# Performance work log

Measured on AMD Instinct MI355X. Metric: run time of the kernel, lower is better.

Reference implementation:

```python
import jax, jax.numpy as jnp
import numpy as np

N_NODES = 80000
N_EDGES = 1280000
IN_C, HID_C, OUT_C = 128, 64, 40


def setup_inputs() -> dict:
    key = jax.random.key(0)
    k1, k2, k3, k4 = jax.random.split(key, 4)
    x = jax.random.normal(k1, (N_NODES, IN_C), dtype=jnp.float32)
    edge_index = jax.random.randint(k2, (2, N_EDGES), 0, N_NODES, dtype=jnp.int32)
    W1 = jax.random.normal(k3, (IN_C, HID_C), dtype=jnp.float32) * (1.0 / np.sqrt(IN_C))
    W2 = jax.random.normal(k4, (HID_C, OUT_C), dtype=jnp.float32) * (1.0 / np.sqrt(HID_C))
    return {"x": x, "edge_index": edge_index, "W1": W1, "W2": W2}


def _spmm_add(edge_index, h):
    # adj_t.matmul(h): out[dst] += h[src]  (aggr='add', message = x_j)
    src, dst = edge_index[0], edge_index[1]
    return jax.ops.segment_sum(h[src], dst, num_segments=N_NODES)


def reference(x, edge_index, W1, W2):
    # GCNConv 1: linear (no bias) then add-aggregate SpMM
    h = _spmm_add(edge_index, x @ W1)          # [N, HID]
    h = jax.nn.relu(h)
    # GCNConv 2
    h = _spmm_add(edge_index, h @ W2)          # [N, OUT]
    return jax.nn.log_softmax(h, axis=-1)
```

## Files before the change

kernel.cpp:

```cpp
#include <hip/hip_runtime.h>
#include <hip/hip_bf16.h>
#include <math.h>

#define N_NODES 80000
#define N_EDGES 1280000
#define IN_C 128
#define HID_C 64
#define OUT_C 40

#define KB 313
#define BK_CAP 4600
#define EPT_A 8

__device__ __forceinline__ float bf_lo(unsigned u) {
    union { unsigned i; float f; } c; c.i = u << 16; return c.f;
}
__device__ __forceinline__ float bf_hi(unsigned u) {
    union { unsigned i; float f; } c; c.i = u & 0xffff0000u; return c.f;
}
__device__ __forceinline__ unsigned pack_bf2(float a, float b) {
    union { float f; unsigned i; } ca, cb; ca.f = a; cb.f = b;
    unsigned ra = (ca.i + 0x7fffu + ((ca.i >> 16) & 1u)) >> 16;
    unsigned rb = (cb.i + 0x7fffu + ((cb.i >> 16) & 1u)) >> 16;
    return ra | (rb << 16);
}

typedef short v8s __attribute__((ext_vector_type(8)));
typedef float v4f __attribute__((ext_vector_type(4)));
typedef float v2f __attribute__((ext_vector_type(2)));
union U16 { uint4 u; v8s s; };

__device__ __forceinline__ v2f bf2f(unsigned u) {
    return (v2f){bf_lo(u), bf_hi(u)};
}
__device__ __forceinline__ void acc_fp8x4(float* a, unsigned u) {
    const v2f lo = __builtin_amdgcn_cvt_pk_f32_fp8((int)u, false);
    const v2f hi = __builtin_amdgcn_cvt_pk_f32_fp8((int)u, true);
    a[0] += lo[0]; a[1] += lo[1]; a[2] += hi[0]; a[3] += hi[1];
}

__global__ void prep_w_kernel(const float* __restrict__ W1, const float* __restrict__ W2,
                              unsigned* __restrict__ w1t, unsigned* __restrict__ w2t,
                              int* __restrict__ bcnt) {
    const int tid = threadIdx.x;
    for (int i = tid; i < KB; i += 256) bcnt[i] = 0;
    for (int i = tid; i < 4096; i += 256) {
        const int wcol = i >> 6, kk = i & 63;
        w1t[i] = pack_bf2(W1[(2 * kk) * HID_C + wcol], W1[(2 * kk + 1) * HID_C + wcol]);
    }
    for (int i = tid; i < 1536; i += 256) {
        const int wcol = i >> 5, kk = i & 31;
        w2t[i] = (wcol < OUT_C)
            ? pack_bf2(W2[(2 * kk) * OUT_C + wcol], W2[(2 * kk + 1) * OUT_C + wcol])
            : 0u;
    }
}

__global__ __launch_bounds__(512) void binA_kernel(const int* __restrict__ src,
                                                   const int* __restrict__ dst,
                                                   int* __restrict__ bcnt,
                                                   int* __restrict__ gbuf) {
    __shared__ int lcnt[KB];
    __shared__ int lexcl[KB];
    __shared__ int lbase[KB];
    __shared__ int lcur[KB];
    __shared__ int stage[512 * EPT_A];
    __shared__ int gaddr[512 * EPT_A];
    const int tid = threadIdx.x;

    for (int i = tid; i < KB; i += 512) lcnt[i] = 0;
    __syncthreads();

    const int e0 = blockIdx.x * 512 * EPT_A;
    int my_s[EPT_A], my_b[EPT_A], my_dl[EPT_A];
#pragma unroll
    for (int j = 0; j < EPT_A; ++j) {
        const int e = e0 + j * 512 + tid;
        if (e < N_EDGES) {
            const int d = dst[e];
            my_s[j] = src[e];
            my_b[j] = d >> 8;
            my_dl[j] = d & 255;
            atomicAdd(&lcnt[my_b[j]], 1);
        } else my_b[j] = -1;
    }
    __syncthreads();

    if (tid < KB) lexcl[tid] = lcnt[tid];
    __syncthreads();
    for (int o = 1; o < KB; o <<= 1) {
        int t = (tid < KB && tid >= o) ? lexcl[tid - o] : 0;
        __syncthreads();
        if (tid < KB) lexcl[tid] += t;
        __syncthreads();
    }
    const int total = lexcl[KB - 1];
    if (tid < KB) {
        lexcl[tid] -= lcnt[tid];
        lbase[tid] = (lcnt[tid] > 0) ? atomicAdd(&bcnt[tid], lcnt[tid]) : 0;
        lcur[tid] = 0;
    }
    __syncthreads();

#pragma unroll
    for (int j = 0; j < EPT_A; ++j) {
        if (my_b[j] >= 0) {
            const int b = my_b[j];
            const int r = atomicAdd(&lcur[b], 1);
            const int li = lexcl[b] + r;
            stage[li] = (my_s[j] << 8) | my_dl[j];
            int gp = lbase[b] + r;
            if (gp >= BK_CAP) gp = BK_CAP - 1;
            gaddr[li] = b * BK_CAP + gp;
        }
    }
    __syncthreads();

    for (int i = tid; i < total; i += 512)
        gbuf[gaddr[i]] = stage[i];
}

__global__ __launch_bounds__(512) void binB_kernel(const int* __restrict__ bcnt,
                                                   const int* __restrict__ gbuf,
                                                   int* __restrict__ rp,
                                                   int* __restrict__ col) {
    __shared__ int sc[KB];
    __shared__ int hist[256];
    __shared__ int excl[256];
    __shared__ int cur[256];
    __shared__ int outb[BK_CAP];
    const int b = blockIdx.x;
    const int tid = threadIdx.x;

    if (tid < KB) sc[tid] = min(bcnt[tid], BK_CAP);
    __syncthreads();
    for (int o = 1; o < KB; o <<= 1) {
        int t = (tid < KB && tid >= o) ? sc[tid - o] : 0;
        __syncthreads();
        if (tid < KB) sc[tid] += t;
        __syncthreads();
    }
    const int n = min(bcnt[b], BK_CAP);
    const int cbase = sc[b] - n;
    const int* __restrict__ my = gbuf + (size_t)b * BK_CAP;

    if (tid < 256) hist[tid] = 0;
    __syncthreads();
    for (int i = tid; i < n; i += 512)
        atomicAdd(&hist[my[i] & 255], 1);
    __syncthreads();

    int h = 0, psv = 0;
    if (tid < 256) { h = hist[tid]; psv = h; excl[tid] = h; }
    __syncthreads();
    for (int o = 1; o < 256; o <<= 1) {
        int t = (tid < 256 && tid >= o) ? excl[tid - o] : 0;
        __syncthreads();
        if (tid < 256) excl[tid] += t;
        __syncthreads();
    }
    if (tid < 256) {
        const int ex = excl[tid] - h;
        cur[tid] = ex;
        const int node = b * 256 + tid;
        if (node <= N_NODES) rp[node] = cbase + ex;
        excl[tid] = ex;
    }
    __syncthreads();

    for (int i = tid; i < n; i += 512) {
        const int pk = my[i];
        const int pos = atomicAdd(&cur[pk & 255], 1);
        outb[pos] = pk >> 8;
    }
    __syncthreads();
    for (int i = tid; i < n; i += 512)
        col[cbase + i] = outb[i];
}

__global__ __launch_bounds__(256) void gemm1_kernel(const float* __restrict__ x,
                                                    const unsigned* __restrict__ w1t,
                                                    unsigned* __restrict__ h1b) {
    const int wave = threadIdx.x >> 6, lane = threadIdx.x & 63;
    const int nl = lane & 15, quad = lane >> 4;
    const int node = (blockIdx.x * 4 + wave) * 16 + nl;

    v4f acc[4];
#pragma unroll
    for (int q = 0; q < 4; ++q) acc[q] = (v4f){0.f, 0.f, 0.f, 0.f};

#pragma unroll
    for (int kit = 0; kit < 4; ++kit) {
        const float* xp = x + (size_t)node * IN_C + kit * 32 + quad * 8;
        const float4 lo = *(const float4*)xp;
        const float4 hi = *(const float4*)(xp + 4);
        U16 bu;
        bu.u.x = pack_bf2(lo.x, lo.y); bu.u.y = pack_bf2(lo.z, lo.w);
        bu.u.z = pack_bf2(hi.x, hi.y); bu.u.w = pack_bf2(hi.z, hi.w);
#pragma unroll
        for (int mt = 0; mt < 4; ++mt) {
            U16 au;
            au.u = *(const uint4*)(w1t + ((mt * 16 + nl) * 64 + kit * 16 + quad * 4));
            acc[mt] = __builtin_amdgcn_mfma_f32_16x16x32_bf16(au.s, bu.s, acc[mt], 0, 0, 0);
        }
    }
#pragma unroll
    for (int mt = 0; mt < 4; ++mt) {
        uint2 o;
        o.x = pack_bf2(acc[mt][0], acc[mt][1]);
        o.y = pack_bf2(acc[mt][2], acc[mt][3]);
        *(uint2*)(h1b + (size_t)node * 32 + mt * 8 + quad * 2) = o;
    }
}

__global__ void gather64_kernel(const int* __restrict__ rp, const int* __restrict__ col,
                                const unsigned* __restrict__ h1b,
                                unsigned* __restrict__ agg1b) {
    const int lane = threadIdx.x & 63;
    const int wave = threadIdx.x >> 6;
    const int sl = lane & 31;
    const int es = sl >> 3;
    const int cl = sl & 7;
    const int gbase = lane & 32;
    const int node = blockIdx.x * 8 + wave * 2 + (lane >> 5);
    const int b = rp[node], e = rp[node + 1];

    v2f acc[4];
#pragma unroll
    for (int k = 0; k < 4; ++k) acc[k] = (v2f){0.f, 0.f};

    for (int pos = b; __any(pos < e); pos += 32) {
        const int rem = e - pos;
        const int n = rem > 32 ? 32 : (rem > 0 ? rem : 0);
        const int myIdx = (sl < n) ? col[pos + sl] : 0;
        const int steps = (n + 3) >> 2;
        int j = 0;
        for (; j + 1 < steps; j += 2) {
            const int e0 = (j << 2) + es, e1 = e0 + 4;
            const int s0 = __shfl(myIdx, gbase + e0, 64);
            const int s1 = __shfl(myIdx, gbase + e1, 64);
            uint4 v0, v1;
            const bool g0 = e0 < n, g1 = e1 < n;
            if (g0) v0 = *(const uint4*)(h1b + (size_t)s0 * 32 + cl * 4);
            if (g1) v1 = *(const uint4*)(h1b + (size_t)s1 * 32 + cl * 4);
            if (g0) {
                acc[0] += bf2f(v0.x); acc[1] += bf2f(v0.y);
                acc[2] += bf2f(v0.z); acc[3] += bf2f(v0.w);
            }
            if (g1) {
                acc[0] += bf2f(v1.x); acc[1] += bf2f(v1.y);
                acc[2] += bf2f(v1.z); acc[3] += bf2f(v1.w);
            }
        }
        if (j < steps) {
            const int e0 = (j << 2) + es;
            const int s0 = __shfl(myIdx, gbase + e0, 64);
            if (e0 < n) {
                const uint4 v = *(const uint4*)(h1b + (size_t)s0 * 32 + cl * 4);
                acc[0] += bf2f(v.x); acc[1] += bf2f(v.y);
                acc[2] += bf2f(v.z); acc[3] += bf2f(v.w);
            }
        }
    }
#pragma unroll
    for (int k = 0; k < 4; ++k) {
        acc[k][0] += __shfl_down(acc[k][0], 16, 64);
        acc[k][1] += __shfl_down(acc[k][1], 16, 64);
    }
#pragma unroll
    for (int k = 0; k < 4; ++k) {
        acc[k][0] += __shfl_down(acc[k][0], 8, 64);
        acc[k][1] += __shfl_down(acc[k][1], 8, 64);
    }

    if (sl < 8) {
        uint4 o;
        o.x = pack_bf2(fmaxf(acc[0][0], 0.f), fmaxf(acc[0][1], 0.f));
        o.y = pack_bf2(fmaxf(acc[1][0], 0.f), fmaxf(acc[1][1], 0.f));
        o.z = pack_bf2(fmaxf(acc[2][0], 0.f), fmaxf(acc[2][1], 0.f));
        o.w = pack_bf2(fmaxf(acc[3][0], 0.f), fmaxf(acc[3][1], 0.f));
        *(uint4*)(agg1b + (size_t)node * 32 + cl * 4) = o;
    }
}

__global__ __launch_bounds__(256) void gemm2_kernel(const unsigned* __restrict__ agg1b,
                                                    const unsigned* __restrict__ w2t,
                                                    unsigned* __restrict__ h2f) {
    const int wave = threadIdx.x >> 6, lane = threadIdx.x & 63;
    const int nl = lane & 15, quad = lane >> 4;
    const int node = (blockIdx.x * 4 + wave) * 16 + nl;

    v4f c[3];
#pragma unroll
    for (int q = 0; q < 3; ++q) c[q] = (v4f){0.f, 0.f, 0.f, 0.f};

#pragma unroll
    for (int kit = 0; kit < 2; ++kit) {
        U16 bu;
        bu.u = *(const uint4*)(agg1b + (size_t)node * 32 + kit * 16 + quad * 4);
#pragma unroll
        for (int mt = 0; mt < 3; ++mt) {
            U16 au;
            au.u = *(const uint4*)(w2t + ((mt * 16 + nl) * 32 + kit * 16 + quad * 4));
            c[mt] = __builtin_amdgcn_mfma_f32_16x16x32_bf16(au.s, bu.s, c[mt], 0, 0, 0);
        }
    }
#pragma unroll
    for (int mt = 0; mt < 3; ++mt) {
        const int idx = mt * 4 + quad;
        if (idx < 10) {
            int u = 0;
            u = __builtin_amdgcn_cvt_pk_fp8_f32(c[mt][0], c[mt][1], u, false);
            u = __builtin_amdgcn_cvt_pk_fp8_f32(c[mt][2], c[mt][3], u, true);
            h2f[(size_t)node * 10 + idx] = (unsigned)u;
        }
    }
}

__global__ void gather40_ls_kernel(const int* __restrict__ rp, const int* __restrict__ col,
                                   const unsigned* __restrict__ h2f,
                                   float* __restrict__ out) {
    const int lane = threadIdx.x & 63;
    const int wave = threadIdx.x >> 6;
    const int sl = lane & 15;
    const int es = sl / 5;
    const int cl = sl - es * 5;
    const int gbase = lane & 48;
    const int node = blockIdx.x * 16 + wave * 4 + (lane >> 4);
    const int b = rp[node], e = rp[node + 1];

    float a[8];
#pragma unroll
    for (int k = 0; k < 8; ++k) a[k] = 0.f;

    for (int pos = b; __any(pos < e); pos += 16) {
        const int rem = e - pos;
        const int n = rem > 16 ? 16 : (rem > 0 ? rem : 0);
        const int myIdx = (sl < n) ? col[pos + sl] : 0;
#pragma unroll
        for (int j = 0; j < 6; ++j) {
            const int ei = j * 3 + es;
            const int s = __shfl(myIdx, gbase + ei, 64);
            if ((es < 3) && (ei < n)) {
                const uint2 v = *(const uint2*)(h2f + (size_t)s * 10 + cl * 2);
                acc_fp8x4(a, v.x);
                acc_fp8x4(a + 4, v.y);
            }
        }
    }
#pragma unroll
    for (int k = 0; k < 8; ++k) {
        const float u = __shfl_down(a[k], 5, 64);
        const float w = __shfl_down(a[k], 10, 64);
        a[k] += u + w;
    }

    const bool own = sl < 5;
    float m = -INFINITY;
    if (own) {
        m = a[0];
#pragma unroll
        for (int k = 1; k < 8; ++k) m = fmaxf(m, a[k]);
    }
    const float m0 = __shfl(m, gbase + 0, 64), m1 = __shfl(m, gbase + 1, 64);
    const float m2 = __shfl(m, gbase + 2, 64), m3 = __shfl(m, gbase + 3, 64);
    const float m4 = __shfl(m, gbase + 4, 64);
    const float gm = fmaxf(fmaxf(fmaxf(m0, m1), fmaxf(m2, m3)), m4);

    float s = 0.f;
    if (own) {
#pragma unroll
        for (int k = 0; k < 8; ++k) s += __expf(a[k] - gm);
    }
    const float s0 = __shfl(s, gbase + 0, 64), s1 = __shfl(s, gbase + 1, 64);
    const float s2 = __shfl(s, gbase + 2, 64), s3 = __shfl(s, gbase + 3, 64);
    const float s4 = __shfl(s, gbase + 4, 64);
    const float ls = __logf(s0 + s1 + s2 + s3 + s4) + gm;

    if (own) {
        float* op = out + (size_t)node * OUT_C + cl * 8;
        *(float4*)op = make_float4(a[0] - ls, a[1] - ls, a[2] - ls, a[3] - ls);
        *(float4*)(op + 4) = make_float4(a[4] - ls, a[5] - ls, a[6] - ls, a[7] - ls);
    }
}

extern "C" void kernel_launch(void* const* d_in, const int* in_sizes, int n_in,
                              void* d_out, int out_size, void* d_ws, size_t ws_size,
                              hipStream_t stream) {
    const float* x  = (const float*)d_in[0];
    const int* eidx = (const int*)d_in[1];
    const float* W1 = (const float*)d_in[2];
    const float* W2 = (const float*)d_in[3];
    float* out = (float*)d_out;

    const int* src = eidx;
    const int* dst = eidx + N_EDGES;

    unsigned* h1b   = (unsigned*)d_ws;
    unsigned* agg1b = h1b + (size_t)N_NODES * 32;
    unsigned* h2f   = agg1b + (size_t)N_NODES * 32;
    int*      gbuf  = (int*)(h2f + (size_t)N_NODES * 10);
    int*      col   = gbuf + (size_t)KB * BK_CAP;
    int*      rp    = col + N_EDGES;
    int*      bcnt  = rp + (N_NODES + 1);
    unsigned* w1t   = (unsigned*)(bcnt + KB);
    unsigned* w2t   = w1t + 4096;

    prep_w_kernel<<<1, 256, 0, stream>>>(W1, W2, w1t, w2t, bcnt);
    binA_kernel<<<(N_EDGES + 512 * EPT_A - 1) / (512 * EPT_A), 512, 0, stream>>>(src, dst, bcnt, gbuf);
    binB_kernel<<<KB, 512, 0, stream>>>(bcnt, gbuf, rp, col);

    gemm1_kernel<<<N_NODES / 64, 256, 0, stream>>>(x, w1t, h1b);
    gather64_kernel<<<N_NODES / 8, 256, 0, stream>>>(rp, col, h1b, agg1b);
    gemm2_kernel<<<N_NODES / 64, 256, 0, stream>>>(agg1b, w2t, h2f);
    gather40_ls_kernel<<<N_NODES / 16, 256, 0, stream>>>(rp, col, h2f, out);
}
```

Baseline: 181.9 us.

## Fuse gemm1 into binning kernel, parallelize weight prep, simplify gather index loads

Merges the first GEMM into the edge-binning launch as extra blocks, so the two independent phases run concurrently and one launch is dropped. Weight preprocessing is spread over 16 blocks instead of one. Both gather kernels now read column indices straight from global memory per edge with a fixed unroll, replacing the cooperative load-and-shuffle. The fused kernel reserves large shared memory for gemm blocks that never use it, which may limit occupancy, and per-lane index loads add redundant memory traffic.

```diff
diff --git a/kernel.cpp b/kernel.cpp
--- a/kernel.cpp
+++ b/kernel.cpp
@@ -11,6 +11,8 @@
 #define KB 313
 #define BK_CAP 4600
 #define EPT_A 8
+#define BINA_BLOCKS 313
+#define GEMM1_BLOCKS 625
 
 __device__ __forceinline__ float bf_lo(unsigned u) {
     union { unsigned i; float f; } c; c.i = u << 16; return c.f;
@@ -33,33 +35,29 @@
 __device__ __forceinline__ v2f bf2f(unsigned u) {
     return (v2f){bf_lo(u), bf_hi(u)};
 }
-__device__ __forceinline__ void acc_fp8x4(float* a, unsigned u) {
-    const v2f lo = __builtin_amdgcn_cvt_pk_f32_fp8((int)u, false);
-    const v2f hi = __builtin_amdgcn_cvt_pk_f32_fp8((int)u, true);
-    a[0] += lo[0]; a[1] += lo[1]; a[2] += hi[0]; a[3] += hi[1];
-}
 
 __global__ void prep_w_kernel(const float* __restrict__ W1, const float* __restrict__ W2,
                               unsigned* __restrict__ w1t, unsigned* __restrict__ w2t,
                               int* __restrict__ bcnt) {
-    const int tid = threadIdx.x;
-    for (int i = tid; i < KB; i += 256) bcnt[i] = 0;
-    for (int i = tid; i < 4096; i += 256) {
-        const int wcol = i >> 6, kk = i & 63;
-        w1t[i] = pack_bf2(W1[(2 * kk) * HID_C + wcol], W1[(2 * kk + 1) * HID_C + wcol]);
-    }
-    for (int i = tid; i < 1536; i += 256) {
-        const int wcol = i >> 5, kk = i & 31;
-        w2t[i] = (wcol < OUT_C)
+    const int g = blockIdx.x * 256 + threadIdx.x;
+    if (g < KB) bcnt[g] = 0;
+    {
+        const int wcol = g >> 6, kk = g & 63;
+        w1t[g] = pack_bf2(W1[(2 * kk) * HID_C + wcol], W1[(2 * kk + 1) * HID_C + wcol]);
+    }
+    if (g < 1536) {
+        const int wcol = g >> 5, kk = g & 31;
+        w2t[g] = (wcol < OUT_C)
             ? pack_bf2(W2[(2 * kk) * OUT_C + wcol], W2[(2 * kk + 1) * OUT_C + wcol])
             : 0u;
     }
 }
 
-__global__ __launch_bounds__(512) void binA_kernel(const int* __restrict__ src,
-                                                   const int* __restrict__ dst,
-                                                   int* __restrict__ bcnt,
-                                                   int* __restrict__ gbuf) {
+__global__ __launch_bounds__(512) void binA_gemm1_kernel(
+        const int* __restrict__ src, const int* __restrict__ dst,
+        int* __restrict__ bcnt, int* __restrict__ gbuf,
+        const float* __restrict__ x, const unsigned* __restrict__ w1t,
+        unsigned* __restrict__ h1b) {
     __shared__ int lcnt[KB];
     __shared__ int lexcl[KB];
     __shared__ int lbase[KB];
@@ -67,6 +65,41 @@
     __shared__ int stage[512 * EPT_A];
     __shared__ int gaddr[512 * EPT_A];
     const int tid = threadIdx.x;
+
+    if (blockIdx.x >= BINA_BLOCKS) {
+        const int bid = blockIdx.x - BINA_BLOCKS;
+        const int wave = tid >> 6, lane = tid & 63;
+        const int nl = lane & 15, quad = lane >> 4;
+        const int node = (bid * 8 + wave) * 16 + nl;
+
+        v4f acc[4];
+#pragma unroll
+        for (int q = 0; q < 4; ++q) acc[q] = (v4f){0.f, 0.f, 0.f, 0.f};
+
+#pragma unroll
+        for (int kit = 0; kit < 4; ++kit) {
+            const float* xp = x + (size_t)node * IN_C + kit * 32 + quad * 8;
+            const float4 lo = *(const float4*)xp;
+            const float4 hi = *(const float4*)(xp + 4);
+            U16 bu;
+            bu.u.x = pack_bf2(lo.x, lo.y); bu.u.y = pack_bf2(lo.z, lo.w);
+            bu.u.z = pack_bf2(hi.x, hi.y); bu.u.w = pack_bf2(hi.z, hi.w);
+#pragma unroll
+            for (int mt = 0; mt < 4; ++mt) {
+                U16 au;
+                au.u = *(const uint4*)(w1t + ((mt * 16 + nl) * 64 + kit * 16 + quad * 4));
+                acc[mt] = __builtin_amdgcn_mfma_f32_16x16x32_bf16(au.s, bu.s, acc[mt], 0, 0, 0);
+            }
+        }
+#pragma unroll
+        for (int mt = 0; mt < 4; ++mt) {
+            uint2 o;
+            o.x = pack_bf2(acc[mt][0], acc[mt][1]);
+            o.y = pack_bf2(acc[mt][2], acc[mt][3]);
+            *(uint2*)(h1b + (size_t)node * 32 + mt * 8 + quad * 2) = o;
+        }
+        return;
+    }
 
     for (int i = tid; i < KB; i += 512) lcnt[i] = 0;
     __syncthreads();
@@ -150,8 +183,8 @@
         atomicAdd(&hist[my[i] & 255], 1);
     __syncthreads();
 
-    int h = 0, psv = 0;
-    if (tid < 256) { h = hist[tid]; psv = h; excl[tid] = h; }
+    int h = 0;
+    if (tid < 256) { h = hist[tid]; excl[tid] = h; }
     __syncthreads();
     for (int o = 1; o < 256; o <<= 1) {
         int t = (tid < 256 && tid >= o) ? excl[tid - o] : 0;
@@ -164,7 +197,6 @@
         cur[tid] = ex;
         const int node = b * 256 + tid;
         if (node <= N_NODES) rp[node] = cbase + ex;
-        excl[tid] = ex;
     }
     __syncthreads();
 
@@ -176,41 +208,6 @@
     __syncthreads();
     for (int i = tid; i < n; i += 512)
         col[cbase + i] = outb[i];
-}
-
-__global__ __launch_bounds__(256) void gemm1_kernel(const float* __restrict__ x,
-                                                    const unsigned* __restrict__ w1t,
-                                                    unsigned* __restrict__ h1b) {
-    const int wave = threadIdx.x >> 6, lane = threadIdx.x & 63;
-    const int nl = lane & 15, quad = lane >> 4;
-    const int node = (blockIdx.x * 4 + wave) * 16 + nl;
-
-    v4f acc[4];
-#pragma unroll
-    for (int q = 0; q < 4; ++q) acc[q] = (v4f){0.f, 0.f, 0.f, 0.f};
-
-#pragma unroll
-    for (int kit = 0; kit < 4; ++kit) {
-        const float* xp = x + (size_t)node * IN_C + kit * 32 + quad * 8;
-        const float4 lo = *(const float4*)xp;
-        const float4 hi = *(const float4*)(xp + 4);
-        U16 bu;
-        bu.u.x = pack_bf2(lo.x, lo.y); bu.u.y = pack_bf2(lo.z, lo.w);
-        bu.u.z = pack_bf2(hi.x, hi.y); bu.u.w = pack_bf2(hi.z, hi.w);
-#pragma unroll
-        for (int mt = 0; mt < 4; ++mt) {
-            U16 au;
-            au.u = *(const uint4*)(w1t + ((mt * 16 + nl) * 64 + kit * 16 + quad * 4));
-            acc[mt] = __builtin_amdgcn_mfma_f32_16x16x32_bf16(au.s, bu.s, acc[mt], 0, 0, 0);
-        }
-    }
-#pragma unroll
-    for (int mt = 0; mt < 4; ++mt) {
-        uint2 o;
-        o.x = pack_bf2(acc[mt][0], acc[mt][1]);
-        o.y = pack_bf2(acc[mt][2], acc[mt][3]);
-        *(uint2*)(h1b + (size_t)node * 32 + mt * 8 + quad * 2) = o;
-    }
 }
 
 __global__ void gather64_kernel(const int* __restrict__ rp, const int* __restrict__ col,
@@ -221,7 +218,6 @@
     const int sl = lane & 31;
     const int es = sl >> 3;
     const int cl = sl & 7;
-    const int gbase = lane & 32;
     const int node = blockIdx.x * 8 + wave * 2 + (lane >> 5);
     const int b = rp[node], e = rp[node + 1];
 
@@ -230,33 +226,12 @@
     for (int k = 0; k < 4; ++k) acc[k] = (v2f){0.f, 0.f};
 
     for (int pos = b; __any(pos < e); pos += 32) {
-        const int rem = e - pos;
-        const int n = rem > 32 ? 32 : (rem > 0 ? rem : 0);
-        const int myIdx = (sl < n) ? col[pos + sl] : 0;
-        const int steps = (n + 3) >> 2;
-        int j = 0;
-        for (; j + 1 < steps; j += 2) {
-            const int e0 = (j << 2) + es, e1 = e0 + 4;
-            const int s0 = __shfl(myIdx, gbase + e0, 64);
-            const int s1 = __shfl(myIdx, gbase + e1, 64);
-            uint4 v0, v1;
-            const bool g0 = e0 < n, g1 = e1 < n;
-            if (g0) v0 = *(const uint4*)(h1b + (size_t)s0 * 32 + cl * 4);
-            if (g1) v1 = *(const uint4*)(h1b + (size_t)s1 * 32 + cl * 4);
-            if (g0) {
-                acc[0] += bf2f(v0.x); acc[1] += bf2f(v0.y);
-                acc[2] += bf2f(v0.z); acc[3] += bf2f(v0.w);
-            }
-            if (g1) {
-                acc[0] += bf2f(v1.x); acc[1] += bf2f(v1.y);
-                acc[2] += bf2f(v1.z); acc[3] += bf2f(v1.w);
-            }
-        }
-        if (j < steps) {
-            const int e0 = (j << 2) + es;
-            const int s0 = __shfl(myIdx, gbase + e0, 64);
-            if (e0 < n) {
-                const uint4 v = *(const uint4*)(h1b + (size_t)s0 * 32 + cl * 4);
+#pragma unroll
+        for (int j = 0; j < 8; ++j) {
+            const int ei = pos + (j << 2) + es;
+            if (ei < e) {
+                const int s = col[ei];
+                const uint4 v = *(const uint4*)(h1b + (size_t)s * 32 + cl * 4);
                 acc[0] += bf2f(v.x); acc[1] += bf2f(v.y);
                 acc[2] += bf2f(v.z); acc[3] += bf2f(v.w);
             }
@@ -329,38 +304,39 @@
     const int node = blockIdx.x * 16 + wave * 4 + (lane >> 4);
     const int b = rp[node], e = rp[node + 1];
 
-    float a[8];
-#pragma unroll
-    for (int k = 0; k < 8; ++k) a[k] = 0.f;
-
-    for (int pos = b; __any(pos < e); pos += 16) {
-        const int rem = e - pos;
-        const int n = rem > 16 ? 16 : (rem > 0 ? rem : 0);
-        const int myIdx = (sl < n) ? col[pos + sl] : 0;
-#pragma unroll
-        for (int j = 0; j < 6; ++j) {
-            const int ei = j * 3 + es;
-            const int s = __shfl(myIdx, gbase + ei, 64);
-            if ((es < 3) && (ei < n)) {
+    v2f a[4];
+#pragma unroll
+    for (int k = 0; k < 4; ++k) a[k] = (v2f){0.f, 0.f};
+
+    for (int pos = b; __any(pos < e); pos += 24) {
+#pragma unroll
+        for (int j = 0; j < 8; ++j) {
+            const int ei = pos + j * 3 + es;
+            if ((es < 3) && (ei < e)) {
+                const int s = col[ei];
                 const uint2 v = *(const uint2*)(h2f + (size_t)s * 10 + cl * 2);
-                acc_fp8x4(a, v.x);
-                acc_fp8x4(a + 4, v.y);
+                a[0] += __builtin_amdgcn_cvt_pk_f32_fp8((int)v.x, false);
+                a[1] += __builtin_amdgcn_cvt_pk_f32_fp8((int)v.x, true);
+                a[2] += __builtin_amdgcn_cvt_pk_f32_fp8((int)v.y, false);
+                a[3] += __builtin_amdgcn_cvt_pk_f32_fp8((int)v.y, true);
             }
         }
     }
 #pragma unroll
-    for (int k = 0; k < 8; ++k) {
-        const float u = __shfl_down(a[k], 5, 64);
-        const float w = __shfl_down(a[k], 10, 64);
-        a[k] += u + w;
+    for (int k = 0; k < 4; ++k) {
+#pragma unroll
+        for (int h = 0; h < 2; ++h) {
+            const float u = __shfl_down(a[k][h], 5, 64);
+            const float w = __shfl_down(a[k][h], 10, 64);
+            a[k][h] += u + w;
+        }
     }
 
     const bool own = sl < 5;
     float m = -INFINITY;
     if (own) {
-        m = a[0];
-#pragma unroll
-        for (int k = 1; k < 8; ++k) m = fmaxf(m, a[k]);
+#pragma unroll
+        for (int k = 0; k < 4; ++k) m = fmaxf(m, fmaxf(a[k][0], a[k][1]));
     }
     const float m0 = __shfl(m, gbase + 0, 64), m1 = __shfl(m, gbase + 1, 64);
     const float m2 = __shfl(m, gbase + 2, 64), m3 = __shfl(m, gbase + 3, 64);
@@ -370,7 +346,8 @@
     float s = 0.f;
     if (own) {
 #pragma unroll
-        for (int k = 0; k < 8; ++k) s += __expf(a[k] - gm);
+        for (int k = 0; k < 4; ++k)
+            s += __expf(a[k][0] - gm) + __expf(a[k][1] - gm);
     }
     const float s0 = __shfl(s, gbase + 0, 64), s1 = __shfl(s, gbase + 1, 64);
     const float s2 = __shfl(s, gbase + 2, 64), s3 = __shfl(s, gbase + 3, 64);
@@ -379,8 +356,8 @@
 
     if (own) {
         float* op = out + (size_t)node * OUT_C + cl * 8;
-        *(float4*)op = make_float4(a[0] - ls, a[1] - ls, a[2] - ls, a[3] - ls);
-        *(float4*)(op + 4) = make_float4(a[4] - ls, a[5] - ls, a[6] - ls, a[7] - ls);
+        *(float4*)op = make_float4(a[0][0] - ls, a[0][1] - ls, a[1][0] - ls, a[1][1] - ls);
+        *(float4*)(op + 4) = make_float4(a[2][0] - ls, a[2][1] - ls, a[3][0] - ls, a[3][1] - ls);
     }
 }
 
@@ -406,11 +383,11 @@
     unsigned* w1t   = (unsigned*)(bcnt + KB);
     unsigned* w2t   = w1t + 4096;
 
-    prep_w_kernel<<<1, 256, 0, stream>>>(W1, W2, w1t, w2t, bcnt);
-    binA_kernel<<<(N_EDGES + 512 * EPT_A - 1) / (512 * EPT_A), 512, 0, stream>>>(src, dst, bcnt, gbuf);
+    prep_w_kernel<<<16, 256, 0, stream>>>(W1, W2, w1t, w2t, bcnt);
+    binA_gemm1_kernel<<<BINA_BLOCKS + GEMM1_BLOCKS, 512, 0, stream>>>(
+        src, dst, bcnt, gbuf, x, w1t, h1b);
     binB_kernel<<<KB, 512, 0, stream>>>(bcnt, gbuf, rp, col);
 
-    gemm1_kernel<<<N_NODES / 64, 256, 0, stream>>>(x, w1t, h1b);
     gather64_kernel<<<N_NODES / 8, 256, 0, stream>>>(rp, col, h1b, agg1b);
     gemm2_kernel<<<N_NODES / 64, 256, 0, stream>>>(agg1b, w2t, h2f);
     gather40_ls_kernel<<<N_NODES / 16, 256, 0, stream>>>(rp, col, h2f, out);
```

Measured after the change: 188.8 us. +3.8%, slower.
